# Kernel tuning notes

Measured on AMD Instinct MI355X. Metric: run time of the kernel, lower is better.

Reference implementation:

```python
import jax, jax.numpy as jnp
import numpy as np

NUM_HEADS = 8
AGENT_NUM = 49
POOL = 7


def _pool_matrix(in_size, out_size):
    # adaptive average pool weights, matches torch AdaptiveAvgPool2d binning
    P = np.zeros((out_size, in_size), np.float32)
    for i in range(out_size):
        s = (i * in_size) // out_size
        e = -((-(i + 1) * in_size) // out_size)
        P[i, s:e] = 1.0 / (e - s)
    return jnp.asarray(P)


def _conv2d(x, w, b, groups=1):
    y = jax.lax.conv_general_dilated(
        x, w, window_strides=(1, 1), padding='SAME',
        dimension_numbers=('NCHW', 'OIHW', 'NCHW'), feature_group_count=groups)
    return y + b[None, :, None, None]


def setup_inputs() -> dict:
    key = jax.random.key(0)
    ks = jax.random.split(key, 16)
    b, n, dim, inner, ctx = 16, 4096, 512, 512, 256
    H = W = cH = cW = 64
    inp = {
        'x': jax.random.normal(ks[0], (b, n, dim), jnp.float32),
        'context': jax.random.normal(ks[1], (b, cH * cW, ctx), jnp.float32),
        'q_w': jax.random.normal(ks[2], (inner, dim), jnp.float32) * 0.02,
        'kv_w': jax.random.normal(ks[3], (2 * inner, dim), jnp.float32) * 0.02,
        'proj_w': jax.random.normal(ks[4], (dim, inner), jnp.float32) * 0.02,
        'proj_b': jax.random.normal(ks[5], (dim,), jnp.float32) * 0.02,
        'conv_w': jax.random.normal(ks[6], (inner, inner + ctx, 3, 3), jnp.float32) * 0.02,
        'conv_b': jax.random.normal(ks[7], (inner,), jnp.float32) * 0.02,
        'dwc_w': jax.random.normal(ks[8], (inner, 1, 3, 3), jnp.float32) * 0.02,
        'dwc_b': jax.random.normal(ks[9], (inner,), jnp.float32) * 0.02,
        'an_bias': jax.random.normal(ks[10], (NUM_HEADS, AGENT_NUM, 7, 7), jnp.float32) * 0.02,
        'na_bias': jax.random.normal(ks[11], (NUM_HEADS, AGENT_NUM, 7, 7), jnp.float32) * 0.02,
        'ah_bias': jax.random.normal(ks[12], (1, NUM_HEADS, AGENT_NUM, H, 1), jnp.float32) * 0.02,
        'aw_bias': jax.random.normal(ks[13], (1, NUM_HEADS, AGENT_NUM, 1, W), jnp.float32) * 0.02,
        'ha_bias': jax.random.normal(ks[14], (1, NUM_HEADS, H, 1, AGENT_NUM), jnp.float32) * 0.02,
        'wa_bias': jax.random.normal(ks[15], (1, NUM_HEADS, 1, W, AGENT_NUM), jnp.float32) * 0.02,
        'H': H, 'W': W, 'c_H': cH, 'c_W': cW,
    }
    return inp


def reference(x, context, q_w, kv_w, proj_w, proj_b, conv_w, conv_b, dwc_w, dwc_b,
              an_bias, na_bias, ah_bias, aw_bias, ha_bias, wa_bias, H, W, c_H, c_W):
    b, n, c = x.shape
    heads, agent_num = NUM_HEADS, AGENT_NUM
    inner = q_w.shape[0]
    ctx_c = context.shape[-1]
    hd = inner // heads
    scale = hd ** (-0.5)

    q = x @ q_w.T                                   # (b, n, inner)
    kv = x @ kv_w.T                                 # (b, n, 2*inner)
    k, v = kv[..., :inner], kv[..., inner:]

    # agent tokens: adaptive-avg-pool q and context to 7x7, concat, 3x3 conv
    Ph, Pw = _pool_matrix(H, POOL), _pool_matrix(W, POOL)
    Pch, Pcw = _pool_matrix(c_H, POOL), _pool_matrix(c_W, POOL)
    pool_x = jnp.einsum('ph,qw,bhwc->bpqc', Ph, Pw, q.reshape(b, H, W, inner)).reshape(b, POOL * POOL, inner)
    pool_ctx = jnp.einsum('ph,qw,bhwc->bpqc', Pch, Pcw, context.reshape(b, c_H, c_W, ctx_c)).reshape(b, POOL * POOL, ctx_c)
    # NOTE: raw reshape (b,49,C)->(b,C,7,7), faithful to the torch code
    agent = jnp.concatenate([pool_x, pool_ctx], axis=2).reshape(b, inner + ctx_c, POOL, POOL)
    agent = _conv2d(agent, conv_w, conv_b).reshape(b, inner, agent_num)
    agent = agent.reshape(b, agent_num, heads, hd).transpose(0, 2, 1, 3)   # (b,h,a,d)

    qh = q.reshape(b, n, heads, hd).transpose(0, 2, 1, 3)  # (b,h,n,d)
    kh = k.reshape(b, n, heads, hd).transpose(0, 2, 1, 3)
    vh = v.reshape(b, n, heads, hd).transpose(0, 2, 1, 3)

    # stage 1: agent -> kv attention
    pb1 = jax.image.resize(an_bias, (heads, agent_num, H, W), method='bilinear').reshape(1, heads, agent_num, n)
    pb2 = (ah_bias + aw_bias).reshape(1, heads, agent_num, n)
    agent_attn = jax.nn.softmax(jnp.einsum('bhad,bhnd->bhan', agent * scale, kh) + pb1 + pb2, axis=-1)
    agent_v = jnp.einsum('bhan,bhnd->bhad', agent_attn, vh)

    # stage 2: query -> agent attention
    ab1 = jax.image.resize(na_bias, (heads, agent_num, H, W), method='bilinear').reshape(1, heads, agent_num, n).transpose(0, 1, 3, 2)
    ab2 = (ha_bias + wa_bias).reshape(1, heads, n, agent_num)
    q_attn = jax.nn.softmax(jnp.einsum('bhnd,bhad->bhna', qh * scale, agent) + ab1 + ab2, axis=-1)
    out = jnp.einsum('bhna,bhad->bhnd', q_attn, agent_v).transpose(0, 2, 1, 3).reshape(b, n, inner)

    # depthwise conv residual on v
    v_img = vh.transpose(0, 2, 1, 3).reshape(b, H, W, inner).transpose(0, 3, 1, 2)
    out = out + _conv2d(v_img, dwc_w, dwc_b, groups=inner).transpose(0, 2, 3, 1).reshape(b, n, inner)

    return out @ proj_w.T + proj_b
```

## Files before the change

### kernel.cpp

```cpp
#include <hip/hip_runtime.h>
#include <cstdint>
#include <cstddef>

#define BB    16
#define NTOK  4096
#define DIMC  512
#define INNER 512
#define CTXC  256
#define HEADS 8
#define HD    64
#define AG    49
#define ASPLIT 8
#define CONVK 6912
#define CKS   16

static const size_t Q_OFF   = 0;
static const size_t KV_OFF  = Q_OFF  + (size_t)BB*NTOK*INNER;
static const size_t A2_OFF  = KV_OFF + (size_t)BB*NTOK*2*INNER;
static const size_t COL_OFF = A2_OFF + (size_t)BB*AG*768;
static const size_t CG_OFF  = COL_OFF+ (size_t)BB*AG*768*9;
static const size_t AGT_OFF = CG_OFF + (size_t)BB*AG*INNER;
static const size_t AGV_OFF = AGT_OFF+ (size_t)BB*HEADS*AG*HD;
static const size_t PB_OFF  = AGV_OFF+ (size_t)BB*HEADS*AG*HD;
static const size_t AB_OFF  = PB_OFF + (size_t)HEADS*AG*NTOK;
static const size_t WSP_OFF = AB_OFF + (size_t)HEADS*NTOK*AG;
static const size_t PNUM_OFF = COL_OFF;
static const size_t PL_OFF   = PNUM_OFF + (size_t)ASPLIT*128*64*64;

typedef __attribute__((ext_vector_type(8))) short  short8;
typedef __attribute__((ext_vector_type(8))) __bf16 bf16x8;
typedef __attribute__((ext_vector_type(4))) float  f32x4;

union SB8 { short8 s; bf16x8 b; };

__device__ inline bf16x8 asbf(short8 v) { SB8 u; u.s = v; return u.b; }

__device__ inline unsigned short bfrn(float x) {
  uint32_t u = __float_as_uint(x);
  return (unsigned short)((u + 0x7FFFu + ((u >> 16) & 1u)) >> 16);
}

struct HL8 { short8 h, l; };

__device__ inline HL8 split8(float4 f0, float4 f1) {
  HL8 r;
  float v0[4] = {f0.x, f0.y, f0.z, f0.w};
  float v1[4] = {f1.x, f1.y, f1.z, f1.w};
#pragma unroll
  for (int j = 0; j < 4; ++j) {
    unsigned short hb = bfrn(v0[j]);
    r.h[j] = (short)hb;
    r.l[j] = (short)bfrn(v0[j] - __uint_as_float((uint32_t)hb << 16));
  }
#pragma unroll
  for (int j = 0; j < 4; ++j) {
    unsigned short hb = bfrn(v1[j]);
    r.h[j + 4] = (short)hb;
    r.l[j + 4] = (short)bfrn(v1[j] - __uint_as_float((uint32_t)hb << 16));
  }
  return r;
}

__device__ inline HL8 split8t(float4 f0, float4 f1) {
  HL8 r;
  float v[8] = {f0.x, f0.y, f0.z, f0.w, f1.x, f1.y, f1.z, f1.w};
#pragma unroll
  for (int j = 0; j < 8; ++j) {
    uint32_t u = __float_as_uint(v[j]);
    uint32_t hb = (u + 0x7FFFu + ((u >> 16) & 1u)) >> 16;
    r.h[j] = (short)hb;
    float res = v[j] - __uint_as_float(hb << 16);
    r.l[j] = (short)(__float_as_uint(res) >> 16);
  }
  return r;
}

__global__ void split_w_kernel(const float* __restrict__ src, short* __restrict__ dhi,
                               short* __restrict__ dlo, int n8) {
  int i = blockIdx.x * 256 + threadIdx.x;
  if (i >= n8) return;
  const float4* s = (const float4*)src + (size_t)i * 2;
  HL8 r = split8(s[0], s[1]);
  *(short8*)(dhi + (size_t)i * 8) = r.h;
  *(short8*)(dlo + (size_t)i * 8) = r.l;
}

#define LSTR 40
template <bool ADD_BIAS>
__global__ __launch_bounds__(256) void gemm_ws3(const float* __restrict__ A,
                                                const short* __restrict__ Bhi_g,
                                                const short* __restrict__ Blo_g,
                                                const float* __restrict__ bias,
                                                float* __restrict__ C,
                                                int M, int Nc, int K) {
  __shared__ short Ahi[128 * LSTR];
  __shared__ short Alo[128 * LSTR];
  __shared__ short Bhi[128 * LSTR];
  __shared__ short Blo[128 * LSTR];
  const int tid  = threadIdx.x;
  const int lane = tid & 63;
  const int wave = tid >> 6;
  const int wm = wave >> 1, wn = wave & 1;
  const int bm = blockIdx.y * 128, bn = blockIdx.x * 128;
  const int srow  = tid >> 1;
  const int shalf = (tid & 1) << 4;
  const int fr  = lane & 15;
  const int fko = (lane >> 4) << 3;

  f32x4 acc[4][4] = {};

  for (int k0 = 0; k0 < K; k0 += 32) {
    {
      const float4* ap = (const float4*)(A + (size_t)(bm + srow) * K + k0 + shalf);
      float4 a0 = ap[0], a1 = ap[1], a2 = ap[2], a3 = ap[3];
      HL8 r0 = split8t(a0, a1);
      *(short8*)&Ahi[srow * LSTR + shalf] = r0.h;
      *(short8*)&Alo[srow * LSTR + shalf] = r0.l;
      HL8 r1 = split8t(a2, a3);
      *(short8*)&Ahi[srow * LSTR + shalf + 8] = r1.h;
      *(short8*)&Alo[srow * LSTR + shalf + 8] = r1.l;
      const short* bhp = Bhi_g + (size_t)(bn + srow) * K + k0 + shalf;
      *(short8*)&Bhi[srow * LSTR + shalf]     = *(const short8*)bhp;
      *(short8*)&Bhi[srow * LSTR + shalf + 8] = *(const short8*)(bhp + 8);
      const short* blp = Blo_g + (size_t)(bn + srow) * K + k0 + shalf;
      *(short8*)&Blo[srow * LSTR + shalf]     = *(const short8*)blp;
      *(short8*)&Blo[srow * LSTR + shalf + 8] = *(const short8*)(blp + 8);
    }
    __syncthreads();
    bf16x8 ah[4], al[4], bh[4], bl[4];
#pragma unroll
    for (int i = 0; i < 4; ++i) {
      int ra = wm * 64 + i * 16 + fr;
      ah[i] = asbf(*(const short8*)&Ahi[ra * LSTR + fko]);
      al[i] = asbf(*(const short8*)&Alo[ra * LSTR + fko]);
      int rb = wn * 64 + i * 16 + fr;
      bh[i] = asbf(*(const short8*)&Bhi[rb * LSTR + fko]);
      bl[i] = asbf(*(const short8*)&Blo[rb * LSTR + fko]);
    }
#pragma unroll
    for (int i = 0; i < 4; ++i)
#pragma unroll
      for (int j = 0; j < 4; ++j) {
        acc[i][j] = __builtin_amdgcn_mfma_f32_16x16x32_bf16(ah[i], bh[j], acc[i][j], 0, 0, 0);
        acc[i][j] = __builtin_amdgcn_mfma_f32_16x16x32_bf16(ah[i], bl[j], acc[i][j], 0, 0, 0);
        acc[i][j] = __builtin_amdgcn_mfma_f32_16x16x32_bf16(al[i], bh[j], acc[i][j], 0, 0, 0);
      }
    __syncthreads();
  }

  const int crow0 = wm * 64 + ((lane >> 4) << 2);
  const int ccol0 = wn * 64 + fr;
  float bs[4];
  if (ADD_BIAS) {
#pragma unroll
    for (int j = 0; j < 4; ++j) bs[j] = bias[bn + ccol0 + j * 16];
  }
#pragma unroll
  for (int i = 0; i < 4; ++i) {
#pragma unroll
    for (int r = 0; r < 4; ++r) {
      size_t row = (size_t)(bm + crow0 + i * 16 + r);
      float* cp = C + row * Nc + bn + ccol0;
#pragma unroll
      for (int j = 0; j < 4; ++j) {
        float v = acc[i][j][r];
        if (ADD_BIAS) v += bs[j];
        cp[j * 16] = v;
      }
    }
  }
}

__global__ void zero_kernel(float* __restrict__ p, int n) {
  int i = blockIdx.x * 256 + threadIdx.x;
  if (i < n) p[i] = 0.f;
}

__global__ __launch_bounds__(256) void conv_gemm_splitk(const float* __restrict__ A,
                                                        const float* __restrict__ Bw,
                                                        float* __restrict__ C) {
  __shared__ float As[16][72];
  __shared__ float Bs[16][72];
  const int tid = threadIdx.x;
  const int tx = tid & 15, ty = tid >> 4;
  const int bn = blockIdx.x * 64;
  const int bm = blockIdx.y * 64;
  const int k_begin = blockIdx.z * (CONVK / CKS);
  const int k_end = k_begin + (CONVK / CKS);
  const int row = tid >> 2, c4 = (tid & 3) << 2;
  float acc[4][4] = {};
  for (int k0 = k_begin; k0 < k_end; k0 += 16) {
    {
      int m = bm + row;
      float4 av = {0.f, 0.f, 0.f, 0.f};
      if (m < 784) av = *(const float4*)(A + (size_t)m * CONVK + k0 + c4);
      As[c4 + 0][row] = av.x; As[c4 + 1][row] = av.y;
      As[c4 + 2][row] = av.z; As[c4 + 3][row] = av.w;
      float4 bv = *(const float4*)(Bw + (size_t)(bn + row) * CONVK + k0 + c4);
      Bs[c4 + 0][row] = bv.x; Bs[c4 + 1][row] = bv.y;
      Bs[c4 + 2][row] = bv.z; Bs[c4 + 3][row] = bv.w;
    }
    __syncthreads();
#pragma unroll
    for (int k = 0; k < 16; ++k) {
      float a[4], b[4];
#pragma unroll
      for (int i = 0; i < 4; ++i) a[i] = As[k][ty * 4 + i];
#pragma unroll
      for (int j = 0; j < 4; ++j) b[j] = Bs[k][tx * 4 + j];
#pragma unroll
      for (int i = 0; i < 4; ++i)
#pragma unroll
        for (int j = 0; j < 4; ++j) acc[i][j] = fmaf(a[i], b[j], acc[i][j]);
    }
    __syncthreads();
  }
#pragma unroll
  for (int i = 0; i < 4; ++i) {
    int m = bm + ty * 4 + i;
    if (m >= 784) continue;
#pragma unroll
    for (int j = 0; j < 4; ++j)
      atomicAdd(C + (size_t)m * INNER + bn + tx * 4 + j, acc[i][j]);
  }
}

__global__ void pool_h_kernel(const float* __restrict__ q, const float* __restrict__ ctx,
                              float* __restrict__ S1q, float* __restrict__ S1c) {
  int idx = blockIdx.x * 256 + threadIdx.x;
  if (idx >= BB * 7 * 64 * 768) return;
  int c  = idx % 768;
  int w  = (idx / 768) & 63;
  int ph = (idx / (768 * 64)) % 7;
  int b  = idx / (768 * 64 * 7);
  int hs = ph * 64 / 7, he = ((ph + 1) * 64 + 6) / 7;
  float s = 0.f;
  if (c < 512) {
    const float* p = q + ((size_t)b * NTOK + hs * 64 + w) * INNER + c;
    for (int h = hs; h < he; ++h) { s += *p; p += 64 * INNER; }
    S1q[((size_t)(b * 7 + ph) * 64 + w) * 512 + c] = s;
  } else {
    int cc = c - 512;
    const float* p = ctx + ((size_t)b * NTOK + hs * 64 + w) * CTXC + cc;
    for (int h = hs; h < he; ++h) { s += *p; p += 64 * CTXC; }
    S1c[((size_t)(b * 7 + ph) * 64 + w) * 256 + cc] = s;
  }
}

__global__ void pool_w_kernel(const float* __restrict__ S1q, const float* __restrict__ S1c,
                              float* __restrict__ A2) {
  int idx = blockIdx.x * 256 + threadIdx.x;
  if (idx >= BB * AG * 768) return;
  int c = idx % 768;
  int p = (idx / 768) % AG;
  int b = idx / (768 * AG);
  int i = p / 7, j = p % 7;
  int hs = i * 64 / 7, he = ((i + 1) * 64 + 6) / 7;
  int ws = j * 64 / 7, we = ((j + 1) * 64 + 6) / 7;
  float inv = 1.f / (float)((he - hs) * (we - ws));
  float s = 0.f;
  if (c < 512) {
    const float* pp = S1q + ((size_t)(b * 7 + i) * 64 + ws) * 512 + c;
    for (int w = ws; w < we; ++w) { s += *pp; pp += 512; }
  } else {
    const float* pp = S1c + ((size_t)(b * 7 + i) * 64 + ws) * 256 + (c - 512);
    for (int w = ws; w < we; ++w) { s += *pp; pp += 256; }
  }
  A2[((size_t)b * AG + p) * 768 + c] = s * inv;
}

__global__ void im2col_kernel(const float* __restrict__ A2, float* __restrict__ Col) {
  int idx = blockIdx.x * 256 + threadIdx.x;
  if (idx >= 784 * 6912) return;
  int r = idx / 6912, t = idx % 6912;
  int ic = t / 9, ky = (t % 9) / 3, kx = t % 3;
  int b = r / AG, p = r % AG;
  int y = p / 7 + ky - 1, x = p % 7 + kx - 1;
  float v = 0.f;
  if (y >= 0 && y < 7 && x >= 0 && x < 7) {
    int g = ic * 49 + y * 7 + x;
    v = A2[((size_t)b * AG + g / 768) * 768 + (g % 768)];
  }
  Col[(size_t)idx] = v;
}

__global__ void agent_scatter_kernel(const float* __restrict__ Cg, const float* __restrict__ conv_b,
                                     float* __restrict__ agent) {
  int idx = blockIdx.x * 256 + threadIdx.x;
  if (idx >= BB * HEADS * AG * HD) return;
  int d = idx & 63;
  int a = (idx >> 6) % AG;
  int h = (idx / (64 * AG)) % HEADS;
  int b = idx / (64 * AG * HEADS);
  int f = a * 512 + h * 64 + d;
  int oc = f / 49, p = f % 49;
  agent[idx] = Cg[((size_t)b * AG + p) * INNER + oc] + conv_b[oc];
}

__device__ inline float bilinear7(const float* __restrict__ Bm, int y, int x) {
  float fy = (y + 0.5f) * (7.f / 64.f) - 0.5f;
  float fx = (x + 0.5f) * (7.f / 64.f) - 0.5f;
  fy = fminf(fmaxf(fy, 0.f), 6.f);
  fx = fminf(fmaxf(fx, 0.f), 6.f);
  int y0 = min((int)floorf(fy), 5);
  int x0 = min((int)floorf(fx), 5);
  float ty = fy - y0, tx = fx - x0;
  float v00 = Bm[y0 * 7 + x0],     v01 = Bm[y0 * 7 + x0 + 1];
  float v10 = Bm[(y0 + 1) * 7 + x0], v11 = Bm[(y0 + 1) * 7 + x0 + 1];
  return (1.f - ty) * ((1.f - tx) * v00 + tx * v01) + ty * ((1.f - tx) * v10 + tx * v11);
}

__global__ void pb_kernel(const float* __restrict__ an_bias, const float* __restrict__ ah,
                          const float* __restrict__ aw, float* __restrict__ pb) {
  int idx = blockIdx.x * 256 + threadIdx.x;
  if (idx >= HEADS * AG * NTOK) return;
  int nn = idx & (NTOK - 1);
  int a = (idx / NTOK) % AG;
  int h = idx / (NTOK * AG);
  int y = nn >> 6, x = nn & 63;
  float v = bilinear7(an_bias + ((size_t)h * AG + a) * 49, y, x);
  v += ah[((size_t)h * AG + a) * 64 + y] + aw[((size_t)h * AG + a) * 64 + x];
  pb[idx] = v;
}

__global__ void ab_kernel(const float* __restrict__ na_bias, const float* __restrict__ ha,
                          const float* __restrict__ wa, float* __restrict__ ab) {
  int idx = blockIdx.x * 256 + threadIdx.x;
  if (idx >= HEADS * NTOK * AG) return;
  int a = idx % AG;
  int nn = (idx / AG) & (NTOK - 1);
  int h = idx / (AG * NTOK);
  int y = nn >> 6, x = nn & 63;
  float v = bilinear7(na_bias + ((size_t)h * AG + a) * 49, y, x);
  v += ha[((size_t)h * 64 + y) * AG + a] + wa[((size_t)h * 64 + x) * AG + a];
  ab[idx] = v;
}

__global__ __launch_bounds__(256, 2) void agent_attn_s(const float* __restrict__ kv,
                                                       const float* __restrict__ agent,
                                                       const float* __restrict__ pb,
                                                       float* __restrict__ part_num,
                                                       float* __restrict__ part_l) {
  const int split = blockIdx.x;
  const int h = blockIdx.y, b = blockIdx.z;
  const int bh = b * HEADS + h;
  __shared__ float agT[64][68];
  __shared__ float ktT[64][68];
  __shared__ float vt[64][68];
  __shared__ float eT[64][68];
  const int tid = threadIdx.x;
  const int tx = tid & 15, ty = tid >> 4;

  for (int idx = tid; idx < AG * 16; idx += 256) {
    int a = idx >> 4, d0 = (idx & 15) << 2;
    float4 v4 = *(const float4*)(agent + ((size_t)bh * AG + a) * HD + d0);
    agT[d0 + 0][a] = v4.x * 0.125f; agT[d0 + 1][a] = v4.y * 0.125f;
    agT[d0 + 2][a] = v4.z * 0.125f; agT[d0 + 3][a] = v4.w * 0.125f;
  }
  for (int idx = tid; idx < 64 * 15; idx += 256) {
    int d = idx / 15, a = AG + idx % 15;
    agT[d][a] = 0.f;
  }

  float accR[4][4] = {};
  float lR[4] = {};

  const float* kb = kv + (size_t)b * NTOK * 1024 + h * 64;
  const float* vb = kb + 512;
  const float* pbh = pb + (size_t)h * AG * NTOK;

  const int nrow = tid & 63, dq = tid >> 6;

  for (int c = 0; c < 8; ++c) {
    const int n0 = split * 512 + c * 64;
#pragma unroll
    for (int i = 0; i < 4; ++i) {
      int d = dq * 16 + i * 4;
      float4 kk = *(const float4*)(kb + (size_t)(n0 + nrow) * 1024 + d);
      ktT[d + 0][nrow] = kk.x; ktT[d + 1][nrow] = kk.y;
      ktT[d + 2][nrow] = kk.z; ktT[d + 3][nrow] = kk.w;
      float4 vv = *(const float4*)(vb + (size_t)(n0 + nrow) * 1024 + d);
      *(float4*)&vt[nrow][d] = vv;
    }
    __syncthreads();
    float s[4][4] = {};
#pragma unroll 4
    for (int d = 0; d < 64; ++d) {
      float4 a4 = *(float4*)&agT[d][ty * 4];
      float4 k4 = *(float4*)&ktT[d][tx * 4];
      s[0][0] = fmaf(a4.x, k4.x, s[0][0]); s[0][1] = fmaf(a4.x, k4.y, s[0][1]);
      s[0][2] = fmaf(a4.x, k4.z, s[0][2]); s[0][3] = fmaf(a4.x, k4.w, s[0][3]);
      s[1][0] = fmaf(a4.y, k4.x, s[1][0]); s[1][1] = fmaf(a4.y, k4.y, s[1][1]);
      s[1][2] = fmaf(a4.y, k4.z, s[1][2]); s[1][3] = fmaf(a4.y, k4.w, s[1][3]);
      s[2][0] = fmaf(a4.z, k4.x, s[2][0]); s[2][1] = fmaf(a4.z, k4.y, s[2][1]);
      s[2][2] = fmaf(a4.z, k4.z, s[2][2]); s[2][3] = fmaf(a4.z, k4.w, s[2][3]);
      s[3][0] = fmaf(a4.w, k4.x, s[3][0]); s[3][1] = fmaf(a4.w, k4.y, s[3][1]);
      s[3][2] = fmaf(a4.w, k4.z, s[3][2]); s[3][3] = fmaf(a4.w, k4.w, s[3][3]);
    }
#pragma unroll
    for (int i = 0; i < 4; ++i) {
      int a = ty * 4 + i;
      int ac = a < AG ? a : AG - 1;
      float4 p4 = *(const float4*)(pbh + (size_t)ac * NTOK + n0 + tx * 4);
      float e0 = __expf(s[i][0] + p4.x);
      float e1 = __expf(s[i][1] + p4.y);
      float e2 = __expf(s[i][2] + p4.z);
      float e3 = __expf(s[i][3] + p4.w);
      lR[i] += e0 + e1 + e2 + e3;
      eT[tx * 4 + 0][a] = e0; eT[tx * 4 + 1][a] = e1;
      eT[tx * 4 + 2][a] = e2; eT[tx * 4 + 3][a] = e3;
    }
    __syncthreads();
#pragma unroll 4
    for (int n = 0; n < 64; ++n) {
      float4 e4 = *(float4*)&eT[n][ty * 4];
      float4 v4 = *(float4*)&vt[n][tx * 4];
      accR[0][0] = fmaf(e4.x, v4.x, accR[0][0]); accR[0][1] = fmaf(e4.x, v4.y, accR[0][1]);
      accR[0][2] = fmaf(e4.x, v4.z, accR[0][2]); accR[0][3] = fmaf(e4.x, v4.w, accR[0][3]);
      accR[1][0] = fmaf(e4.y, v4.x, accR[1][0]); accR[1][1] = fmaf(e4.y, v4.y, accR[1][1]);
      accR[1][2] = fmaf(e4.y, v4.z, accR[1][2]); accR[1][3] = fmaf(e4.y, v4.w, accR[1][3]);
      accR[2][0] = fmaf(e4.z, v4.x, accR[2][0]); accR[2][1] = fmaf(e4.z, v4.y, accR[2][1]);
      accR[2][2] = fmaf(e4.z, v4.z, accR[2][2]); accR[2][3] = fmaf(e4.z, v4.w, accR[2][3]);
      accR[3][0] = fmaf(e4.w, v4.x, accR[3][0]); accR[3][1] = fmaf(e4.w, v4.y, accR[3][1]);
      accR[3][2] = fmaf(e4.w, v4.z, accR[3][2]); accR[3][3] = fmaf(e4.w, v4.w, accR[3][3]);
    }
    __syncthreads();
  }
#pragma unroll
  for (int i = 0; i < 4; ++i) {
    float l = lR[i];
    l += __shfl_xor(l, 1, 64); l += __shfl_xor(l, 2, 64);
    l += __shfl_xor(l, 4, 64); l += __shfl_xor(l, 8, 64);
    lR[i] = l;
  }
  float* pn = part_num + ((size_t)(split * 128 + bh)) * 64 * 64;
  float* pl = part_l + (size_t)(split * 128 + bh) * 64;
#pragma unroll
  for (int i = 0; i < 4; ++i) {
    int a = ty * 4 + i;
    if (a < AG) {
      float4 o = {accR[i][0], accR[i][1], accR[i][2], accR[i][3]};
      *(float4*)(pn + a * 64 + tx * 4) = o;
      if (tx == 0) pl[a] = lR[i];
    }
  }
}

__global__ void agent_attn_combine(const float* __restrict__ part_num,
                                   const float* __restrict__ part_l,
                                   float* __restrict__ agent_v) {
  int idx = blockIdx.x * 256 + threadIdx.x;
  if (idx >= 128 * AG * 64) return;
  int d = idx & 63;
  int a = (idx >> 6) % AG;
  int bh = idx / (AG * 64);
  float num = 0.f, l = 0.f;
#pragma unroll
  for (int s = 0; s < ASPLIT; ++s) {
    num += part_num[((size_t)(s * 128 + bh)) * 4096 + a * 64 + d];
    l += part_l[(size_t)(s * 128 + bh) * 64 + a];
  }
  agent_v[((size_t)bh * AG + a) * HD + d] = num / l;
}

__global__ __launch_bounds__(256) void q_attn_kernel(const float* __restrict__ agent,
                                                     const float* __restrict__ agent_v,
                                                     const float* __restrict__ ab,
                                                     float* __restrict__ q) {
  const int tile = blockIdx.x;
  const int h = blockIdx.y, b = blockIdx.z;
  __shared__ float ag[AG][HD];
  __shared__ float av[AG][HD];
  const int tid = threadIdx.x;
  const size_t base = ((size_t)(b * HEADS + h)) * AG * HD;
  for (int t = tid; t < AG * HD; t += 256) {
    ag[t / HD][t % HD] = agent[base + t] * 0.125f;
    av[t / HD][t % HD] = agent_v[base + t];
  }
  __syncthreads();
  const int nn = tile * 256 + tid;
  float* qrow = q + ((size_t)(b * NTOK) + nn) * INNER + h * 64;
  float qr[64];
#pragma unroll
  for (int d = 0; d < 64; d += 4) {
    float4 v4 = *(const float4*)(qrow + d);
    qr[d] = v4.x; qr[d + 1] = v4.y; qr[d + 2] = v4.z; qr[d + 3] = v4.w;
  }
  const float* abr = ab + ((size_t)h * NTOK + nn) * AG;
  float scr[AG];
  float m = -3.4e38f;
  for (int a = 0; a < AG; ++a) {
    float dot = 0.f;
#pragma unroll
    for (int d = 0; d < 64; ++d) dot = fmaf(qr[d], ag[a][d], dot);
    float s = dot + abr[a];
    scr[a] = s;
    m = fmaxf(m, s);
  }
  float l = 0.f;
  for (int a = 0; a < AG; ++a) {
    float e = __expf(scr[a] - m);
    scr[a] = e;
    l += e;
  }
  const float invl = 1.f / l;
#pragma unroll
  for (int d = 0; d < 64; ++d) qr[d] = 0.f;
  for (int a = 0; a < AG; ++a) {
    float p = scr[a] * invl;
#pragma unroll
    for (int d = 0; d < 64; ++d) qr[d] = fmaf(p, av[a][d], qr[d]);
  }
#pragma unroll
  for (int d = 0; d < 64; d += 4) {
    float4 v4 = {qr[d], qr[d + 1], qr[d + 2], qr[d + 3]};
    *(float4*)(qrow + d) = v4;
  }
}

__global__ __launch_bounds__(256) void dwc4_kernel(const float* __restrict__ kv,
                                                   const float* __restrict__ dwc_w,
                                                   const float* __restrict__ dwc_b,
                                                   float* __restrict__ outp) {
  int idx = blockIdx.x * 256 + threadIdx.x;
  int cq = (idx & 127) << 2;
  int r  = idx >> 7;
  int x = r & 63, y = (r >> 6) & 63, b = r >> 12;
  float wreg[36];
  {
    const float4* wp = (const float4*)(dwc_w + (size_t)cq * 9);
#pragma unroll
    for (int j = 0; j < 9; ++j) {
      float4 t = wp[j];
      wreg[4 * j + 0] = t.x; wreg[4 * j + 1] = t.y;
      wreg[4 * j + 2] = t.z; wreg[4 * j + 3] = t.w;
    }
  }
  float4 s = *(const float4*)(dwc_b + cq);
  const float* vb = kv + (size_t)b * NTOK * 1024 + 512 + cq;
#pragma unroll
  for (int ky = 0; ky < 3; ++ky) {
    int yy = y + ky - 1;
    if (yy < 0 || yy > 63) continue;
#pragma unroll
    for (int kx = 0; kx < 3; ++kx) {
      int xx = x + kx - 1;
      if (xx < 0 || xx > 63) continue;
      float4 v4 = *(const float4*)(vb + (size_t)(yy * 64 + xx) * 1024);
      const int t = ky * 3 + kx;
      s.x = fmaf(wreg[0 * 9 + t], v4.x, s.x);
      s.y = fmaf(wreg[1 * 9 + t], v4.y, s.y);
      s.z = fmaf(wreg[2 * 9 + t], v4.z, s.z);
      s.w = fmaf(wreg[3 * 9 + t], v4.w, s.w);
    }
  }
  size_t o = (size_t)r * INNER + cq;
  float4 cur = *(const float4*)(outp + o);
  cur.x += s.x; cur.y += s.y; cur.z += s.z; cur.w += s.w;
  *(float4*)(outp + o) = cur;
}

extern "C" void kernel_launch(void* const* d_in, const int* in_sizes, int n_in,
                              void* d_out, int out_size, void* d_ws, size_t ws_size,
                              hipStream_t stream) {
  const float* x       = (const float*)d_in[0];
  const float* context = (const float*)d_in[1];
  const float* q_w     = (const float*)d_in[2];
  const float* kv_w    = (const float*)d_in[3];
  const float* proj_w  = (const float*)d_in[4];
  const float* proj_b  = (const float*)d_in[5];
  const float* conv_w  = (const float*)d_in[6];
  const float* conv_b  = (const float*)d_in[7];
  const float* dwc_w   = (const float*)d_in[8];
  const float* dwc_b   = (const float*)d_in[9];
  const float* an_bias = (const float*)d_in[10];
  const float* na_bias = (const float*)d_in[11];
  const float* ah_bias = (const float*)d_in[12];
  const float* aw_bias = (const float*)d_in[13];
  const float* ha_bias = (const float*)d_in[14];
  const float* wa_bias = (const float*)d_in[15];
  float* out = (float*)d_out;
  float* wsf = (float*)d_ws;

  float* q_buf  = wsf + Q_OFF;
  float* kv_buf = wsf + KV_OFF;
  float* A2     = wsf + A2_OFF;
  float* Col    = wsf + COL_OFF;
  float* Cg     = wsf + CG_OFF;
  float* agent  = wsf + AGT_OFF;
  float* agentv = wsf + AGV_OFF;
  float* pb     = wsf + PB_OFF;
  float* ab     = wsf + AB_OFF;
  float* pnum   = wsf + PNUM_OFF;
  float* pl     = wsf + PL_OFF;
  short* whi    = (short*)(wsf + WSP_OFF);
  short* wlo    = whi + (size_t)2048 * 512;
  float* S1q    = wsf + COL_OFF;
  float* S1c    = wsf + CG_OFF;

  const int M = BB * NTOK;

  split_w_kernel<<<(512 * 512 / 8 + 255) / 256, 256, 0, stream>>>(q_w, whi, wlo, 512 * 512 / 8);
  split_w_kernel<<<(1024 * 512 / 8 + 255) / 256, 256, 0, stream>>>(kv_w, whi + (size_t)512 * 512, wlo + (size_t)512 * 512, 1024 * 512 / 8);
  split_w_kernel<<<(512 * 512 / 8 + 255) / 256, 256, 0, stream>>>(proj_w, whi + (size_t)1536 * 512, wlo + (size_t)1536 * 512, 512 * 512 / 8);

  gemm_ws3<false><<<dim3(INNER / 128, M / 128), 256, 0, stream>>>(x, whi, wlo, nullptr, q_buf, M, INNER, DIMC);
  gemm_ws3<false><<<dim3(2 * INNER / 128, M / 128), 256, 0, stream>>>(x, whi + (size_t)512 * 512, wlo + (size_t)512 * 512, nullptr, kv_buf, M, 2 * INNER, DIMC);
  pool_h_kernel<<<(BB * 7 * 64 * 768) / 256, 256, 0, stream>>>(q_buf, context, S1q, S1c);
  pool_w_kernel<<<(BB * AG * 768 + 255) / 256, 256, 0, stream>>>(S1q, S1c, A2);
  im2col_kernel<<<(784 * 6912 + 255) / 256, 256, 0, stream>>>(A2, Col);
  zero_kernel<<<(784 * INNER + 255) / 256, 256, 0, stream>>>(Cg, 784 * INNER);
  conv_gemm_splitk<<<dim3(INNER / 64, (784 + 63) / 64, CKS), 256, 0, stream>>>(Col, conv_w, Cg);
  agent_scatter_kernel<<<(BB * HEADS * AG * HD + 255) / 256, 256, 0, stream>>>(Cg, conv_b, agent);
  pb_kernel<<<(HEADS * AG * NTOK + 255) / 256, 256, 0, stream>>>(an_bias, ah_bias, aw_bias, pb);
  ab_kernel<<<(HEADS * NTOK * AG + 255) / 256, 256, 0, stream>>>(na_bias, ha_bias, wa_bias, ab);
  agent_attn_s<<<dim3(ASPLIT, HEADS, BB), 256, 0, stream>>>(kv_buf, agent, pb, pnum, pl);
  agent_attn_combine<<<(128 * AG * 64 + 255) / 256, 256, 0, stream>>>(pnum, pl, agentv);
  q_attn_kernel<<<dim3(NTOK / 256, HEADS, BB), 256, 0, stream>>>(agent, agentv, ab, q_buf);
  dwc4_kernel<<<(BB * NTOK * 128) / 256, 256, 0, stream>>>(kv_buf, dwc_w, dwc_b, q_buf);
  gemm_ws3<true><<<dim3(DIMC / 128, M / 128), 256, 0, stream>>>(q_buf, whi + (size_t)1536 * 512, wlo + (size_t)1536 * 512, proj_b, out, M, DIMC, INNER);

  (void)in_sizes; (void)n_in; (void)out_size; (void)ws_size;
}
```

Baseline: 1.578 ms.

## Use split-bf16 MFMA for query-agent attention and merge Q/KV projection GEMMs

The scalar-FMA q_attn kernel is replaced by an MFMA version. It splits operands into hi/lo bf16 pairs, computes the scores and softmax in registers, and stages the probabilities through LDS for the second matmul. The agent_v combine kernel now writes transposed hi/lo bf16 buffers padded to 64 agents. The Q and KV projections are fused into a single GEMM launch that routes output column tiles to two buffers, with a workgroup-index swizzle added for cache locality. The intent is to cut scalar ALU time in q_attn and launch overhead, at the cost of three-pass bf16 accuracy and a bit of padding work.

```diff
diff --git a/kernel.cpp b/kernel.cpp
--- a/kernel.cpp
+++ b/kernel.cpp
@@ -26,6 +26,7 @@
 static const size_t WSP_OFF = AB_OFF + (size_t)HEADS*NTOK*AG;
 static const size_t PNUM_OFF = COL_OFF;
 static const size_t PL_OFF   = PNUM_OFF + (size_t)ASPLIT*128*64*64;
+static const size_t AVT_OFF  = PL_OFF + (size_t)ASPLIT*128*64;
 
 typedef __attribute__((ext_vector_type(8))) short  short8;
 typedef __attribute__((ext_vector_type(8))) __bf16 bf16x8;
@@ -91,8 +92,9 @@
                                                 const short* __restrict__ Bhi_g,
                                                 const short* __restrict__ Blo_g,
                                                 const float* __restrict__ bias,
-                                                float* __restrict__ C,
-                                                int M, int Nc, int K) {
+                                                float* __restrict__ C1, int nc1,
+                                                float* __restrict__ C2, int nc2,
+                                                int M, int K) {
   __shared__ short Ahi[128 * LSTR];
   __shared__ short Alo[128 * LSTR];
   __shared__ short Bhi[128 * LSTR];
@@ -101,7 +103,11 @@
   const int lane = tid & 63;
   const int wave = tid >> 6;
   const int wm = wave >> 1, wn = wave & 1;
-  const int bm = blockIdx.y * 128, bn = blockIdx.x * 128;
+  const int nwg = gridDim.x * gridDim.y;
+  const int lin = blockIdx.y * gridDim.x + blockIdx.x;
+  const int swz = (lin & 7) * (nwg >> 3) + (lin >> 3);
+  const int bx = swz % gridDim.x, by = swz / gridDim.x;
+  const int bm = by * 128, bnT = bx * 128;
   const int srow  = tid >> 1;
   const int shalf = (tid & 1) << 4;
   const int fr  = lane & 15;
@@ -119,10 +125,10 @@
       HL8 r1 = split8t(a2, a3);
       *(short8*)&Ahi[srow * LSTR + shalf + 8] = r1.h;
       *(short8*)&Alo[srow * LSTR + shalf + 8] = r1.l;
-      const short* bhp = Bhi_g + (size_t)(bn + srow) * K + k0 + shalf;
+      const short* bhp = Bhi_g + (size_t)(bnT + srow) * K + k0 + shalf;
       *(short8*)&Bhi[srow * LSTR + shalf]     = *(const short8*)bhp;
       *(short8*)&Bhi[srow * LSTR + shalf + 8] = *(const short8*)(bhp + 8);
-      const short* blp = Blo_g + (size_t)(bn + srow) * K + k0 + shalf;
+      const short* blp = Blo_g + (size_t)(bnT + srow) * K + k0 + shalf;
       *(short8*)&Blo[srow * LSTR + shalf]     = *(const short8*)blp;
       *(short8*)&Blo[srow * LSTR + shalf + 8] = *(const short8*)(blp + 8);
     }
@@ -150,17 +156,20 @@
 
   const int crow0 = wm * 64 + ((lane >> 4) << 2);
   const int ccol0 = wn * 64 + fr;
+  float* Cb; int ncb, coff;
+  if (bnT < nc1) { Cb = C1; ncb = nc1; coff = bnT; }
+  else           { Cb = C2; ncb = nc2; coff = bnT - nc1; }
   float bs[4];
   if (ADD_BIAS) {
 #pragma unroll
-    for (int j = 0; j < 4; ++j) bs[j] = bias[bn + ccol0 + j * 16];
+    for (int j = 0; j < 4; ++j) bs[j] = bias[bnT + ccol0 + j * 16];
   }
 #pragma unroll
   for (int i = 0; i < 4; ++i) {
 #pragma unroll
     for (int r = 0; r < 4; ++r) {
       size_t row = (size_t)(bm + crow0 + i * 16 + r);
-      float* cp = C + row * Nc + bn + ccol0;
+      float* cp = Cb + row * ncb + coff + ccol0;
 #pragma unroll
       for (int j = 0; j < 4; ++j) {
         float v = acc[i][j][r];
@@ -448,74 +457,185 @@
 
 __global__ void agent_attn_combine(const float* __restrict__ part_num,
                                    const float* __restrict__ part_l,
-                                   float* __restrict__ agent_v) {
+                                   short* __restrict__ avThi, short* __restrict__ avTlo) {
   int idx = blockIdx.x * 256 + threadIdx.x;
-  if (idx >= 128 * AG * 64) return;
-  int d = idx & 63;
-  int a = (idx >> 6) % AG;
-  int bh = idx / (AG * 64);
-  float num = 0.f, l = 0.f;
-#pragma unroll
-  for (int s = 0; s < ASPLIT; ++s) {
-    num += part_num[((size_t)(s * 128 + bh)) * 4096 + a * 64 + d];
-    l += part_l[(size_t)(s * 128 + bh) * 64 + a];
-  }
-  agent_v[((size_t)bh * AG + a) * HD + d] = num / l;
-}
-
-__global__ __launch_bounds__(256) void q_attn_kernel(const float* __restrict__ agent,
-                                                     const float* __restrict__ agent_v,
-                                                     const float* __restrict__ ab,
-                                                     float* __restrict__ q) {
+  if (idx >= 128 * 64 * 64) return;
+  int a = idx & 63;
+  int d = (idx >> 6) & 63;
+  int bh = idx >> 12;
+  float v = 0.f;
+  if (a < AG) {
+    float num = 0.f, l = 0.f;
+#pragma unroll
+    for (int s = 0; s < ASPLIT; ++s) {
+      num += part_num[((size_t)(s * 128 + bh)) * 4096 + a * 64 + d];
+      l += part_l[(size_t)(s * 128 + bh) * 64 + a];
+    }
+    v = num / l;
+  }
+  unsigned short hb = bfrn(v);
+  float res = v - __uint_as_float((uint32_t)hb << 16);
+  avThi[(size_t)bh * 4096 + d * 64 + a] = (short)hb;
+  avTlo[(size_t)bh * 4096 + d * 64 + a] = (short)(__float_as_uint(res) >> 16);
+}
+
+#define PSTR 80
+__global__ __launch_bounds__(256) void q_attn_mfma(const float* __restrict__ agent,
+                                                   const short* __restrict__ avThi,
+                                                   const short* __restrict__ avTlo,
+                                                   const float* __restrict__ ab,
+                                                   float* __restrict__ q) {
   const int tile = blockIdx.x;
   const int h = blockIdx.y, b = blockIdx.z;
-  __shared__ float ag[AG][HD];
-  __shared__ float av[AG][HD];
+  const int bh = b * HEADS + h;
+  __shared__ short Phi[128 * PSTR];
+  __shared__ short Plo[128 * PSTR];
   const int tid = threadIdx.x;
-  const size_t base = ((size_t)(b * HEADS + h)) * AG * HD;
-  for (int t = tid; t < AG * HD; t += 256) {
-    ag[t / HD][t % HD] = agent[base + t] * 0.125f;
-    av[t / HD][t % HD] = agent_v[base + t];
-  }
+  const int lane = tid & 63;
+  const int wave = tid >> 6;
+  const int woff = wave * 32;
+  const int fr = lane & 15;
+  const int fko = (lane >> 4) << 3;
+  const int rg = lane >> 4;
+
+  const size_t agbase = (size_t)bh * AG * HD;
+  const int gtok0 = tile * 128 + woff;
+  const size_t qrow0 = (size_t)b * NTOK + gtok0;
+
+  bf16x8 agh[2][4], agl[2][4];
+#pragma unroll
+  for (int j = 0; j < 4; ++j) {
+    int ar = j * 16 + fr; if (ar > AG - 1) ar = AG - 1;
+#pragma unroll
+    for (int kh = 0; kh < 2; ++kh) {
+      const float4* p = (const float4*)(agent + agbase + (size_t)ar * HD + kh * 32 + fko);
+      float4 f0 = p[0], f1 = p[1];
+      f0.x *= 0.125f; f0.y *= 0.125f; f0.z *= 0.125f; f0.w *= 0.125f;
+      f1.x *= 0.125f; f1.y *= 0.125f; f1.z *= 0.125f; f1.w *= 0.125f;
+      HL8 r = split8t(f0, f1);
+      agh[kh][j] = asbf(r.h); agl[kh][j] = asbf(r.l);
+    }
+  }
+
+  bf16x8 qh_[2][2], ql_[2][2];
+#pragma unroll
+  for (int i = 0; i < 2; ++i)
+#pragma unroll
+    for (int kh = 0; kh < 2; ++kh) {
+      const float4* p = (const float4*)(q + (qrow0 + i * 16 + fr) * INNER + h * 64 + kh * 32 + fko);
+      HL8 r = split8t(p[0], p[1]);
+      qh_[i][kh] = asbf(r.h); ql_[i][kh] = asbf(r.l);
+    }
+
+  f32x4 sa[2][4] = {};
+#pragma unroll
+  for (int i = 0; i < 2; ++i)
+#pragma unroll
+    for (int j = 0; j < 4; ++j)
+#pragma unroll
+      for (int kh = 0; kh < 2; ++kh) {
+        sa[i][j] = __builtin_amdgcn_mfma_f32_16x16x32_bf16(qh_[i][kh], agh[kh][j], sa[i][j], 0, 0, 0);
+        sa[i][j] = __builtin_amdgcn_mfma_f32_16x16x32_bf16(qh_[i][kh], agl[kh][j], sa[i][j], 0, 0, 0);
+        sa[i][j] = __builtin_amdgcn_mfma_f32_16x16x32_bf16(ql_[i][kh], agh[kh][j], sa[i][j], 0, 0, 0);
+      }
+
+  float ev[2][4][4];
+  float lsum[2][4];
+#pragma unroll
+  for (int i = 0; i < 2; ++i) {
+#pragma unroll
+    for (int r = 0; r < 4; ++r) {
+      int t = gtok0 + i * 16 + 4 * rg + r;
+      const float* abp = ab + ((size_t)h * NTOK + t) * AG;
+      float sv[4];
+      float m = -3.4e38f;
+#pragma unroll
+      for (int j = 0; j < 4; ++j) {
+        int a = j * 16 + fr;
+        int ac = a < AG ? a : AG - 1;
+        float xv = sa[i][j][r] + abp[ac];
+        sv[j] = (a < AG) ? xv : -3.4e38f;
+        m = fmaxf(m, sv[j]);
+      }
+      m = fmaxf(m, __shfl_xor(m, 1, 64));
+      m = fmaxf(m, __shfl_xor(m, 2, 64));
+      m = fmaxf(m, __shfl_xor(m, 4, 64));
+      m = fmaxf(m, __shfl_xor(m, 8, 64));
+      float l = 0.f;
+#pragma unroll
+      for (int j = 0; j < 4; ++j) {
+        int a = j * 16 + fr;
+        float e = (a < AG) ? __expf(sv[j] - m) : 0.f;
+        ev[i][j][r] = e;
+        l += e;
+      }
+      l += __shfl_xor(l, 1, 64);
+      l += __shfl_xor(l, 2, 64);
+      l += __shfl_xor(l, 4, 64);
+      l += __shfl_xor(l, 8, 64);
+      lsum[i][r] = l;
+    }
+  }
+
+#pragma unroll
+  for (int i = 0; i < 2; ++i)
+#pragma unroll
+    for (int r = 0; r < 4; ++r) {
+      int lt = woff + i * 16 + 4 * rg + r;
+#pragma unroll
+      for (int j = 0; j < 4; ++j) {
+        int a = j * 16 + fr;
+        float e = ev[i][j][r];
+        unsigned short hb = bfrn(e);
+        float res = e - __uint_as_float((uint32_t)hb << 16);
+        Phi[lt * PSTR + a] = (short)hb;
+        Plo[lt * PSTR + a] = (short)(__float_as_uint(res) >> 16);
+      }
+    }
   __syncthreads();
-  const int nn = tile * 256 + tid;
-  float* qrow = q + ((size_t)(b * NTOK) + nn) * INNER + h * 64;
-  float qr[64];
-#pragma unroll
-  for (int d = 0; d < 64; d += 4) {
-    float4 v4 = *(const float4*)(qrow + d);
-    qr[d] = v4.x; qr[d + 1] = v4.y; qr[d + 2] = v4.z; qr[d + 3] = v4.w;
-  }
-  const float* abr = ab + ((size_t)h * NTOK + nn) * AG;
-  float scr[AG];
-  float m = -3.4e38f;
-  for (int a = 0; a < AG; ++a) {
-    float dot = 0.f;
-#pragma unroll
-    for (int d = 0; d < 64; ++d) dot = fmaf(qr[d], ag[a][d], dot);
-    float s = dot + abr[a];
-    scr[a] = s;
-    m = fmaxf(m, s);
-  }
-  float l = 0.f;
-  for (int a = 0; a < AG; ++a) {
-    float e = __expf(scr[a] - m);
-    scr[a] = e;
-    l += e;
-  }
-  const float invl = 1.f / l;
-#pragma unroll
-  for (int d = 0; d < 64; ++d) qr[d] = 0.f;
-  for (int a = 0; a < AG; ++a) {
-    float p = scr[a] * invl;
-#pragma unroll
-    for (int d = 0; d < 64; ++d) qr[d] = fmaf(p, av[a][d], qr[d]);
-  }
-#pragma unroll
-  for (int d = 0; d < 64; d += 4) {
-    float4 v4 = {qr[d], qr[d + 1], qr[d + 2], qr[d + 3]};
-    *(float4*)(qrow + d) = v4;
-  }
+
+  const short* avhp = avThi + (size_t)bh * 4096;
+  const short* avlp = avTlo + (size_t)bh * 4096;
+  bf16x8 vh_[2][4], vl_[2][4];
+#pragma unroll
+  for (int j = 0; j < 4; ++j)
+#pragma unroll
+    for (int kh = 0; kh < 2; ++kh) {
+      size_t o = (size_t)(j * 16 + fr) * 64 + kh * 32 + fko;
+      vh_[kh][j] = asbf(*(const short8*)(avhp + o));
+      vl_[kh][j] = asbf(*(const short8*)(avlp + o));
+    }
+  bf16x8 ph_[2][2], pl_[2][2];
+#pragma unroll
+  for (int i = 0; i < 2; ++i)
+#pragma unroll
+    for (int kh = 0; kh < 2; ++kh) {
+      int lt = woff + i * 16 + fr;
+      ph_[i][kh] = asbf(*(const short8*)&Phi[lt * PSTR + kh * 32 + fko]);
+      pl_[i][kh] = asbf(*(const short8*)&Plo[lt * PSTR + kh * 32 + fko]);
+    }
+  f32x4 oa[2][4] = {};
+#pragma unroll
+  for (int i = 0; i < 2; ++i)
+#pragma unroll
+    for (int j = 0; j < 4; ++j)
+#pragma unroll
+      for (int kh = 0; kh < 2; ++kh) {
+        oa[i][j] = __builtin_amdgcn_mfma_f32_16x16x32_bf16(ph_[i][kh], vh_[kh][j], oa[i][j], 0, 0, 0);
+        oa[i][j] = __builtin_amdgcn_mfma_f32_16x16x32_bf16(ph_[i][kh], vl_[kh][j], oa[i][j], 0, 0, 0);
+        oa[i][j] = __builtin_amdgcn_mfma_f32_16x16x32_bf16(pl_[i][kh], vh_[kh][j], oa[i][j], 0, 0, 0);
+      }
+
+#pragma unroll
+  for (int i = 0; i < 2; ++i)
+#pragma unroll
+    for (int r = 0; r < 4; ++r) {
+      float inv = 1.f / lsum[i][r];
+      float* qp = q + (qrow0 + i * 16 + 4 * rg + r) * INNER + h * 64;
+#pragma unroll
+      for (int j = 0; j < 4; ++j)
+        qp[j * 16 + fr] = oa[i][j][r] * inv;
+    }
 }
 
 __global__ __launch_bounds__(256) void dwc4_kernel(const float* __restrict__ kv,
@@ -588,11 +708,12 @@
   float* Col    = wsf + COL_OFF;
   float* Cg     = wsf + CG_OFF;
   float* agent  = wsf + AGT_OFF;
-  float* agentv = wsf + AGV_OFF;
   float* pb     = wsf + PB_OFF;
   float* ab     = wsf + AB_OFF;
   float* pnum   = wsf + PNUM_OFF;
   float* pl     = wsf + PL_OFF;
+  short* avThi  = (short*)(wsf + AVT_OFF);
+  short* avTlo  = avThi + (size_t)128 * 64 * 64;
   short* whi    = (short*)(wsf + WSP_OFF);
   short* wlo    = whi + (size_t)2048 * 512;
   float* S1q    = wsf + COL_OFF;
@@ -604,8 +725,8 @@
   split_w_kernel<<<(1024 * 512 / 8 + 255) / 256, 256, 0, stream>>>(kv_w, whi + (size_t)512 * 512, wlo + (size_t)512 * 512, 1024 * 512 / 8);
   split_w_kernel<<<(512 * 512 / 8 + 255) / 256, 256, 0, stream>>>(proj_w, whi + (size_t)1536 * 512, wlo + (size_t)1536 * 512, 512 * 512 / 8);
 
-  gemm_ws3<false><<<dim3(INNER / 128, M / 128), 256, 0, stream>>>(x, whi, wlo, nullptr, q_buf, M, INNER, DIMC);
-  gemm_ws3<false><<<dim3(2 * INNER / 128, M / 128), 256, 0, stream>>>(x, whi + (size_t)512 * 512, wlo + (size_t)512 * 512, nullptr, kv_buf, M, 2 * INNER, DIMC);
+  gemm_ws3<false><<<dim3(1536 / 128, M / 128), 256, 0, stream>>>(x, whi, wlo, nullptr,
+                                                                 q_buf, INNER, kv_buf, 2 * INNER, M, DIMC);
   pool_h_kernel<<<(BB * 7 * 64 * 768) / 256, 256, 0, stream>>>(q_buf, context, S1q, S1c);
   pool_w_kernel<<<(BB * AG * 768 + 255) / 256, 256, 0, stream>>>(S1q, S1c, A2);
   im2col_kernel<<<(784 * 6912 + 255) / 256, 256, 0, stream>>>(A2, Col);
@@ -615,10 +736,11 @@
   pb_kernel<<<(HEADS * AG * NTOK + 255) / 256, 256, 0, stream>>>(an_bias, ah_bias, aw_bias, pb);
   ab_kernel<<<(HEADS * NTOK * AG + 255) / 256, 256, 0, stream>>>(na_bias, ha_bias, wa_bias, ab);
   agent_attn_s<<<dim3(ASPLIT, HEADS, BB), 256, 0, stream>>>(kv_buf, agent, pb, pnum, pl);
-  agent_attn_combine<<<(128 * AG * 64 + 255) / 256, 256, 0, stream>>>(pnum, pl, agentv);
-  q_attn_kernel<<<dim3(NTOK / 256, HEADS, BB), 256, 0, stream>>>(agent, agentv, ab, q_buf);
+  agent_attn_combine<<<(128 * 64 * 64) / 256, 256, 0, stream>>>(pnum, pl, avThi, avTlo);
+  q_attn_mfma<<<dim3(NTOK / 128, HEADS, BB), 256, 0, stream>>>(agent, avThi, avTlo, ab, q_buf);
   dwc4_kernel<<<(BB * NTOK * 128) / 256, 256, 0, stream>>>(kv_buf, dwc_w, dwc_b, q_buf);
-  gemm_ws3<true><<<dim3(DIMC / 128, M / 128), 256, 0, stream>>>(q_buf, whi + (size_t)1536 * 512, wlo + (size_t)1536 * 512, proj_b, out, M, DIMC, INNER);
+  gemm_ws3<true><<<dim3(DIMC / 128, M / 128), 256, 0, stream>>>(q_buf, whi + (size_t)1536 * 512, wlo + (size_t)1536 * 512,
+                                                                proj_b, out, DIMC, out, 0, M, INNER);
 
   (void)in_sizes; (void)n_in; (void)out_size; (void)ws_size;
 }
```

Measured after the change: 1.434 ms. 1.1x faster.
